# Kernel tuning notes

Measured on AMD Instinct MI355X. Metric: run time of the kernel, lower is better.

## Reference

```python
import jax, jax.numpy as jnp
import numpy as np

N_USERS = 10000
RESERVE = 100
N_TOTAL = N_USERS + RESERVE  # 10100 graph nodes (incl. unknown-user slots)
D = 128                      # user_id_embedding_size
B = 2048                     # batch of user ids
AVG_DEG = 32


def _build_friendship_matrix(rng: np.random.Generator) -> np.ndarray:
    # Dense symmetric friendship matrix with 1.0 on the diagonal (self-loop),
    # mirroring torch.diag(ones) + symmetric weighted edge insertion.
    F = np.zeros((N_TOTAL, N_TOTAL), dtype=np.float32)
    np.fill_diagonal(F, 1.0)
    n_edges = N_USERS * AVG_DEG // 2
    src = rng.integers(0, N_USERS, size=n_edges)
    dst = rng.integers(0, N_USERS, size=n_edges)
    w = rng.uniform(0.1, 1.0, size=n_edges).astype(np.float32)
    F[src, dst] = w
    F[dst, src] = w
    return F


def setup_inputs() -> dict:
    key = jax.random.key(0)
    k_ids, k_emb, k_w, k_b = jax.random.split(key, 4)
    rng = np.random.default_rng(0)
    user_ids = jax.random.randint(k_ids, (B,), 0, N_USERS, dtype=jnp.int32)
    friendship_matrix = jnp.asarray(_build_friendship_matrix(rng))      # (N, N)
    # torch init: embeddings ~ U[0,1); Linear weight/bias ~ U[-1/sqrt(d), 1/sqrt(d)]
    user_id_embeddings = jax.random.uniform(k_emb, (N_TOTAL, D), dtype=jnp.float32)
    bound = 1.0 / np.sqrt(D)
    lin_weight = jax.random.uniform(k_w, (D, D), minval=-bound, maxval=bound, dtype=jnp.float32)
    lin_bias = jax.random.uniform(k_b, (D,), minval=-bound, maxval=bound, dtype=jnp.float32)
    return {
        "user_ids": user_ids,
        "friendship_matrix": friendship_matrix,
        "user_id_embeddings": user_id_embeddings,
        "lin_weight": lin_weight,
        "lin_bias": lin_bias,
    }


def reference(user_ids, friendship_matrix, user_id_embeddings, lin_weight, lin_bias):
    # Per user: friends = F[uid]; aggregated = sum_n friends[n] * E[n]
    # Vectorized over the batch: gather rows of F, then one GEMM with E.
    friends = friendship_matrix[user_ids]                 # (B, N)
    aggregated = friends @ user_id_embeddings             # (B, D)
    # torch.nn.Linear: x @ W^T + b
    return aggregated @ lin_weight.T + lin_bias           # (B, D)
```

## Files before the change

kernel.cpp:

```cpp
#include <hip/hip_runtime.h>


#define NTOT 10100
#define NV4  2525
#define DIM  128
#define CAP  1024
#define TPB  512
#define NGRP 4

__global__ __launch_bounds__(TPB) void friendship_kernel(
    const int*   __restrict__ uids,
    const float* __restrict__ F,
    const float* __restrict__ E,
    const float* __restrict__ W,
    const float* __restrict__ bias,
    float*       __restrict__ out)
{
    __shared__ int   s_idx[CAP];
    __shared__ float s_w[CAP];
    __shared__ int   s_cnt;
    __shared__ float s_red[TPB];
    __shared__ float s_agg[DIM];
    __shared__ float s_out[DIM];

    const int row = blockIdx.x;
    const int tid = threadIdx.x;
    const int uid = uids[row];
    const float* Frow = F + (size_t)uid * NTOT;

    if (tid == 0) s_cnt = 0;
    __syncthreads();

    const float4* Frow4 = (const float4*)Frow;
    for (int i = tid; i < NV4; i += TPB) {
        float4 v = Frow4[i];
        int n = i * 4;
        bool ba = v.x != 0.0f, bb = v.y != 0.0f, bc = v.z != 0.0f, bd = v.w != 0.0f;
        int  m  = (int)ba + (int)bb + (int)bc + (int)bd;
        if (m) {
            int p = atomicAdd(&s_cnt, m);
            if (p + m <= CAP) {
                if (ba) { s_idx[p] = n;     s_w[p] = v.x; ++p; }
                if (bb) { s_idx[p] = n + 1; s_w[p] = v.y; ++p; }
                if (bc) { s_idx[p] = n + 2; s_w[p] = v.z; ++p; }
                if (bd) { s_idx[p] = n + 3; s_w[p] = v.w; ++p; }
            }
        }
    }
    __syncthreads();

    const int cnt = s_cnt;
    const int d   = tid & (DIM - 1);
    const int g   = tid >> 7;

    float acc = 0.0f;
    if (cnt <= CAP) {
        int k = g;
        for (; k + 3 * NGRP < cnt; k += 4 * NGRP) {
            int   n0 = s_idx[k],            n1 = s_idx[k +     NGRP];
            int   n2 = s_idx[k + 2 * NGRP], n3 = s_idx[k + 3 * NGRP];
            float w0 = s_w[k],              w1 = s_w[k +     NGRP];
            float w2 = s_w[k + 2 * NGRP],   w3 = s_w[k + 3 * NGRP];
            acc += w0 * E[(size_t)n0 * DIM + d];
            acc += w1 * E[(size_t)n1 * DIM + d];
            acc += w2 * E[(size_t)n2 * DIM + d];
            acc += w3 * E[(size_t)n3 * DIM + d];
        }
        for (; k < cnt; k += NGRP)
            acc += s_w[k] * E[(size_t)s_idx[k] * DIM + d];
    } else {
        for (int n = g; n < NTOT; n += NGRP)
            acc += Frow[n] * E[(size_t)n * DIM + d];
    }
    s_red[tid] = acc;
    __syncthreads();
    if (tid < DIM)
        s_agg[tid] = s_red[tid] + s_red[tid + DIM] + s_red[tid + 2 * DIM] + s_red[tid + 3 * DIM];
    __syncthreads();

    const float4* W4 = (const float4*)W;
    #pragma unroll
    for (int q = 0; q < 8; ++q) {
        int i4 = tid + TPB * q;
        float4 wv = W4[i4];
        int dd = (i4 & 31) * 4;
        float p = wv.x * s_agg[dd]     + wv.y * s_agg[dd + 1]
                + wv.z * s_agg[dd + 2] + wv.w * s_agg[dd + 3];
        p += __shfl_xor(p, 16);
        p += __shfl_xor(p, 8);
        p += __shfl_xor(p, 4);
        p += __shfl_xor(p, 2);
        p += __shfl_xor(p, 1);
        if ((tid & 31) == 0) s_out[i4 >> 5] = p;
    }
    __syncthreads();
    if (tid < DIM)
        out[(size_t)row * DIM + tid] = bias[tid] + s_out[tid];
}

extern "C" void kernel_launch(void* const* d_in, const int* in_sizes, int n_in,
                              void* d_out, int out_size, void* d_ws, size_t ws_size,
                              hipStream_t stream) {
    const int*   uids = (const int*)  d_in[0];
    const float* F    = (const float*)d_in[1];
    const float* E    = (const float*)d_in[2];
    const float* W    = (const float*)d_in[3];
    const float* bias = (const float*)d_in[4];
    float*       out  = (float*)d_out;

    const int B = in_sizes[0];
    friendship_kernel<<<B, TPB, 0, stream>>>(uids, F, E, W, bias, out);
}
```

Before: 30.70 us.

## Compact nonzeros per wavefront with ballot/popcount instead of shared atomics

Each of four wavefronts scans a quarter of the friendship row and compacts nonzeros into its own shared list using ballot and popcount prefix sums, which removes the shared-memory atomic counter and one block barrier. Each wavefront then gathers embedding rows for its own neighbors with float2 loads per lane and writes a partial sum. The partials are reduced across wavefronts. Block size drops from 512 to 256 threads. The per-wave capacity of 80 sends dense quarters to a slower fallback path, and there are fewer threads to hide gather latency.

```diff
diff --git a/kernel.cpp b/kernel.cpp
--- a/kernel.cpp
+++ b/kernel.cpp
@@ -3,10 +3,10 @@
 
 #define NTOT 10100
 #define NV4  2525
+#define QV4  632
 #define DIM  128
-#define CAP  1024
-#define TPB  512
-#define NGRP 4
+#define WCAP 80
+#define TPB  256
 
 __global__ __launch_bounds__(TPB) void friendship_kernel(
     const int*   __restrict__ uids,
@@ -16,82 +16,106 @@
     const float* __restrict__ bias,
     float*       __restrict__ out)
 {
-    __shared__ int   s_idx[CAP];
-    __shared__ float s_w[CAP];
-    __shared__ int   s_cnt;
-    __shared__ float s_red[TPB];
+    __shared__ int   s_idx[4][WCAP];
+    __shared__ float s_w[4][WCAP];
+    __shared__ float s_part[4][DIM];
     __shared__ float s_agg[DIM];
     __shared__ float s_out[DIM];
 
-    const int row = blockIdx.x;
-    const int tid = threadIdx.x;
-    const int uid = uids[row];
+    const int row  = blockIdx.x;
+    const int tid  = threadIdx.x;
+    const int w    = tid >> 6;
+    const int lane = tid & 63;
+    const int uid  = uids[row];
     const float* Frow = F + (size_t)uid * NTOT;
+    const float4* Frow4 = (const float4*)Frow;
 
-    if (tid == 0) s_cnt = 0;
-    __syncthreads();
+    const int jbeg = w * QV4;
+    const int jend = (w == 3) ? NV4 : (jbeg + QV4);
+    const unsigned long long below = (1ULL << lane) - 1ULL;
+    const int nrounds = (jend - jbeg + 63) >> 6;
 
-    const float4* Frow4 = (const float4*)Frow;
-    for (int i = tid; i < NV4; i += TPB) {
-        float4 v = Frow4[i];
-        int n = i * 4;
-        bool ba = v.x != 0.0f, bb = v.y != 0.0f, bc = v.z != 0.0f, bd = v.w != 0.0f;
-        int  m  = (int)ba + (int)bb + (int)bc + (int)bd;
-        if (m) {
-            int p = atomicAdd(&s_cnt, m);
-            if (p + m <= CAP) {
-                if (ba) { s_idx[p] = n;     s_w[p] = v.x; ++p; }
-                if (bb) { s_idx[p] = n + 1; s_w[p] = v.y; ++p; }
-                if (bc) { s_idx[p] = n + 2; s_w[p] = v.z; ++p; }
-                if (bd) { s_idx[p] = n + 3; s_w[p] = v.w; ++p; }
+    int cb = 0;
+    for (int t = 0; t < nrounds; ++t) {
+        const int j = jbeg + t * 64 + lane;
+        float4 v = make_float4(0.f, 0.f, 0.f, 0.f);
+        if (j < jend) v = Frow4[j];
+        bool b0 = v.x != 0.0f, b1 = v.y != 0.0f, b2 = v.z != 0.0f, b3 = v.w != 0.0f;
+        unsigned long long m0 = __ballot(b0), m1 = __ballot(b1);
+        unsigned long long m2 = __ballot(b2), m3 = __ballot(b3);
+        if (m0 | m1 | m2 | m3) {
+            int t0 = __popcll(m0), t1 = __popcll(m1), t2 = __popcll(m2);
+            int n = j * 4;
+            int p0 = cb + __popcll(m0 & below);
+            int p1 = cb + t0 + __popcll(m1 & below);
+            int p2 = cb + t0 + t1 + __popcll(m2 & below);
+            int p3 = cb + t0 + t1 + t2 + __popcll(m3 & below);
+            if (b0 && p0 < WCAP) { s_idx[w][p0] = n;     s_w[w][p0] = v.x; }
+            if (b1 && p1 < WCAP) { s_idx[w][p1] = n + 1; s_w[w][p1] = v.y; }
+            if (b2 && p2 < WCAP) { s_idx[w][p2] = n + 2; s_w[w][p2] = v.z; }
+            if (b3 && p3 < WCAP) { s_idx[w][p3] = n + 3; s_w[w][p3] = v.w; }
+            cb += t0 + t1 + t2 + __popcll(m3);
+        }
+    }
+    asm volatile("s_waitcnt lgkmcnt(0)" ::: "memory");
+    __builtin_amdgcn_sched_barrier(0);
+
+    float2 acc = make_float2(0.0f, 0.0f);
+    const float* Ed = E + 2 * lane;
+    if (cb <= WCAP) {
+        int k = 0;
+        for (; k + 4 <= cb; k += 4) {
+            int   n0 = s_idx[w][k],     n1 = s_idx[w][k + 1];
+            int   n2 = s_idx[w][k + 2], n3 = s_idx[w][k + 3];
+            float w0 = s_w[w][k],       w1 = s_w[w][k + 1];
+            float w2 = s_w[w][k + 2],   w3 = s_w[w][k + 3];
+            float2 e0 = *(const float2*)(Ed + (size_t)n0 * DIM);
+            float2 e1 = *(const float2*)(Ed + (size_t)n1 * DIM);
+            float2 e2 = *(const float2*)(Ed + (size_t)n2 * DIM);
+            float2 e3 = *(const float2*)(Ed + (size_t)n3 * DIM);
+            acc.x += w0 * e0.x; acc.y += w0 * e0.y;
+            acc.x += w1 * e1.x; acc.y += w1 * e1.y;
+            acc.x += w2 * e2.x; acc.y += w2 * e2.y;
+            acc.x += w3 * e3.x; acc.y += w3 * e3.y;
+        }
+        for (; k < cb; ++k) {
+            int   n = s_idx[w][k];
+            float ww = s_w[w][k];
+            float2 ev = *(const float2*)(Ed + (size_t)n * DIM);
+            acc.x += ww * ev.x; acc.y += ww * ev.y;
+        }
+    } else {
+        int nbeg = jbeg * 4, nend = (w == 3) ? NTOT : (jend * 4);
+        for (int n = nbeg; n < nend; ++n) {
+            float fw = Frow[n];
+            if (fw != 0.0f) {
+                float2 ev = *(const float2*)(Ed + (size_t)n * DIM);
+                acc.x += fw * ev.x; acc.y += fw * ev.y;
             }
         }
     }
+    *(float2*)&s_part[w][2 * lane] = acc;
     __syncthreads();
 
-    const int cnt = s_cnt;
-    const int d   = tid & (DIM - 1);
-    const int g   = tid >> 7;
-
-    float acc = 0.0f;
-    if (cnt <= CAP) {
-        int k = g;
-        for (; k + 3 * NGRP < cnt; k += 4 * NGRP) {
-            int   n0 = s_idx[k],            n1 = s_idx[k +     NGRP];
-            int   n2 = s_idx[k + 2 * NGRP], n3 = s_idx[k + 3 * NGRP];
-            float w0 = s_w[k],              w1 = s_w[k +     NGRP];
-            float w2 = s_w[k + 2 * NGRP],   w3 = s_w[k + 3 * NGRP];
-            acc += w0 * E[(size_t)n0 * DIM + d];
-            acc += w1 * E[(size_t)n1 * DIM + d];
-            acc += w2 * E[(size_t)n2 * DIM + d];
-            acc += w3 * E[(size_t)n3 * DIM + d];
-        }
-        for (; k < cnt; k += NGRP)
-            acc += s_w[k] * E[(size_t)s_idx[k] * DIM + d];
-    } else {
-        for (int n = g; n < NTOT; n += NGRP)
-            acc += Frow[n] * E[(size_t)n * DIM + d];
-    }
-    s_red[tid] = acc;
-    __syncthreads();
     if (tid < DIM)
-        s_agg[tid] = s_red[tid] + s_red[tid + DIM] + s_red[tid + 2 * DIM] + s_red[tid + 3 * DIM];
+        s_agg[tid] = s_part[0][tid] + s_part[1][tid] + s_part[2][tid] + s_part[3][tid];
     __syncthreads();
 
     const float4* W4 = (const float4*)W;
     #pragma unroll
-    for (int q = 0; q < 8; ++q) {
+    for (int q = 0; q < 16; ++q) {
         int i4 = tid + TPB * q;
         float4 wv = W4[i4];
+        int j  = i4 >> 5;
         int dd = (i4 & 31) * 4;
-        float p = wv.x * s_agg[dd]     + wv.y * s_agg[dd + 1]
-                + wv.z * s_agg[dd + 2] + wv.w * s_agg[dd + 3];
+        float4 ag = *(const float4*)&s_agg[dd];
+        float p = wv.x * ag.x + wv.y * ag.y + wv.z * ag.z + wv.w * ag.w;
         p += __shfl_xor(p, 16);
         p += __shfl_xor(p, 8);
         p += __shfl_xor(p, 4);
         p += __shfl_xor(p, 2);
         p += __shfl_xor(p, 1);
-        if ((tid & 31) == 0) s_out[i4 >> 5] = p;
+        if ((tid & 31) == 0) s_out[j] = p;
     }
     __syncthreads();
     if (tid < DIM)
```

Measured after the change: 37.06 us. 1.21x slower.
